# Kernel optimization log

Measured on AMD Instinct MI355X. Metric: run time of the kernel, lower is better.

Reference implementation:

```python
import jax, jax.numpy as jnp
import numpy as np

B, Q, C, H, D, E, I = 8, 256, 192, 20, 64, 1500, 5120
HID = H * D  # 1280
EPS = 1e-5
SCALE = D ** -0.5


def _linear(x, w, b):
    return jnp.einsum('bsh,oh->bso', x, w) + b


def _layernorm(x, w, b):
    xf = x.astype(jnp.float32)
    mu = jnp.mean(xf, axis=-1, keepdims=True)
    var = jnp.mean(jnp.square(xf - mu), axis=-1, keepdims=True)
    return ((xf - mu) * jax.lax.rsqrt(var + EPS) * w + b).astype(x.dtype)


def _heads(x):  # [B,S,HID] -> [B,H,S,D]
    return x.reshape(B, -1, H, D).transpose(0, 2, 1, 3)


def setup_inputs() -> dict:
    key = jax.random.key(0)
    ks = jax.random.split(key, 24)
    s = 0.02
    inp = {
        'hidden_states': jax.random.normal(ks[0], (B, Q, HID), jnp.float32),
        'mask': jnp.zeros((B, 1, Q, Q + C), jnp.float32),
        'past_key': jax.random.normal(ks[1], (B, H, C, D), jnp.float32),
        'past_value': jax.random.normal(ks[2], (B, H, C, D), jnp.float32),
        'cross_key': jax.random.normal(ks[3], (B, H, E, D), jnp.float32),
        'cross_value': jax.random.normal(ks[4], (B, H, E, D), jnp.float32),
        'q_w': jax.random.normal(ks[5], (HID, HID), jnp.float32) * s,
        'q_b': jnp.zeros((HID,), jnp.float32),
        'k_w': jax.random.normal(ks[6], (HID, HID), jnp.float32) * s,
        'k_b': jnp.zeros((HID,), jnp.float32),
        'v_w': jax.random.normal(ks[7], (HID, HID), jnp.float32) * s,
        'v_b': jnp.zeros((HID,), jnp.float32),
        'o_w': jax.random.normal(ks[8], (HID, HID), jnp.float32) * s,
        'o_b': jnp.zeros((HID,), jnp.float32),
        'cq_w': jax.random.normal(ks[9], (HID, HID), jnp.float32) * s,
        'cq_b': jnp.zeros((HID,), jnp.float32),
        'co_w': jax.random.normal(ks[10], (HID, HID), jnp.float32) * s,
        'co_b': jnp.zeros((HID,), jnp.float32),
        'up_w': jax.random.normal(ks[11], (I, HID), jnp.float32) * s,
        'up_b': jnp.zeros((I,), jnp.float32),
        'down_w': jax.random.normal(ks[12], (HID, I), jnp.float32) * s,
        'down_b': jnp.zeros((HID,), jnp.float32),
        'ln1_w': jnp.ones((HID,), jnp.float32),
        'ln1_b': jnp.zeros((HID,), jnp.float32),
        'ln2_w': jnp.ones((HID,), jnp.float32),
        'ln2_b': jnp.zeros((HID,), jnp.float32),
        'ln3_w': jnp.ones((HID,), jnp.float32),
        'ln3_b': jnp.zeros((HID,), jnp.float32),
    }
    return inp


def reference(hidden_states, mask, past_key, past_value, cross_key, cross_value,
              q_w, q_b, k_w, k_b, v_w, v_b, o_w, o_b,
              cq_w, cq_b, co_w, co_b, up_w, up_b, down_w, down_b,
              ln1_w, ln1_b, ln2_w, ln2_b, ln3_w, ln3_b):
    # ---- self-attention block ----
    residual = hidden_states
    x = _layernorm(hidden_states, ln1_w, ln1_b)
    q = _heads(_linear(x, q_w, q_b) * SCALE)          # [B,H,Q,D]
    k_new = _heads(_linear(x, k_w, k_b))              # [B,H,Q,D]
    v_new = _heads(_linear(x, v_w, v_b))
    k = jnp.concatenate([past_key, k_new], axis=2)    # [B,H,C+Q,D]
    v = jnp.concatenate([past_value, v_new], axis=2)
    scores = jnp.einsum('bhqd,bhkd->bhqk', q, k) + mask
    attn = jnp.einsum('bhqk,bhkd->bhqd', jax.nn.softmax(scores, axis=-1), v)
    attn = attn.transpose(0, 2, 1, 3).reshape(B, Q, HID)
    attn_out = _linear(attn, o_w, o_b)
    present_key = k[:, :, Q:, :]
    present_value = v[:, :, Q:, :]
    h = residual + attn_out
    # ---- cross-attention block ----
    residual = h
    x = _layernorm(h, ln2_w, ln2_b)
    cq = _heads(_linear(x, cq_w, cq_b) * SCALE)       # [B,H,Q,D]
    cscores = jnp.einsum('bhqd,bhkd->bhqk', cq, cross_key)
    cattn = jnp.einsum('bhqk,bhkd->bhqd', jax.nn.softmax(cscores, axis=-1), cross_value)
    cattn = cattn.transpose(0, 2, 1, 3).reshape(B, Q, HID)
    h = residual + _linear(cattn, co_w, co_b)
    # ---- MLP block ----
    residual = h
    x = _layernorm(h, ln3_w, ln3_b)
    up = _linear(x, up_w, up_b)
    mlp_out = _linear(jax.nn.gelu(up, approximate=False), down_w, down_b)
    h = residual + mlp_out
    return (h, present_key, present_value)
```

## Files before the change

kernel.cpp:

```cpp
#include <hip/hip_runtime.h>
#include <math.h>

#define Bc   8
#define Qn   256
#define Cn   192
#define Hn   20
#define Dn   64
#define En   1500
#define In   5120
#define HIDn 1280
#define BQ   2048
#define KSELF 448
#define S1   (BQ*HIDn)
#define WSZ  (HIDn*HIDn)

typedef __attribute__((ext_vector_type(8))) short bf16x8;
typedef __attribute__((ext_vector_type(4))) float f32x4;

__device__ __forceinline__ short f2bf(float f) {
  union { float f; unsigned u; } x; x.f = f;
  unsigned r = x.u + 0x7fffu + ((x.u >> 16) & 1u);
  return (short)(r >> 16);
}
__device__ __forceinline__ float bf2f(short s) {
  union { unsigned u; float f; } x; x.u = ((unsigned)(unsigned short)s) << 16;
  return x.f;
}
__device__ __forceinline__ void gload16(const short* g, short* l) {
  __builtin_amdgcn_global_load_lds(
      (const __attribute__((address_space(1))) void*)g,
      (__attribute__((address_space(3))) void*)l, 16, 0, 0);
}

__global__ __launch_bounds__(256) void convert_all(
    const float* q, const float* k, const float* v, const float* o,
    const float* cq, const float* co, const float* up, const float* dn,
    short* wq, short* wk, short* wv, short* wo,
    short* wcq, short* wco, short* wup, short* wdn)
{
  const float* src; short* dst; int n;
  switch (blockIdx.y) {
    case 0: src = q;  dst = wq;  n = WSZ; break;
    case 1: src = k;  dst = wk;  n = WSZ; break;
    case 2: src = v;  dst = wv;  n = WSZ; break;
    case 3: src = o;  dst = wo;  n = WSZ; break;
    case 4: src = cq; dst = wcq; n = WSZ; break;
    case 5: src = co; dst = wco; n = WSZ; break;
    case 6: src = up; dst = wup; n = HIDn * In; break;
    default: src = dn; dst = wdn; n = HIDn * In; break;
  }
  const int i = (blockIdx.x * 256 + threadIdx.x) * 8;
  if (i >= n) return;
  const float4 a = *reinterpret_cast<const float4*>(src + i);
  const float4 b = *reinterpret_cast<const float4*>(src + i + 4);
  bf16x8 t;
  t[0] = f2bf(a.x); t[1] = f2bf(a.y); t[2] = f2bf(a.z); t[3] = f2bf(a.w);
  t[4] = f2bf(b.x); t[5] = f2bf(b.y); t[6] = f2bf(b.z); t[7] = f2bf(b.w);
  *reinterpret_cast<bf16x8*>(dst + i) = t;
}

__global__ __launch_bounds__(256) void layernorm_k(
    const float* __restrict__ in, const float* __restrict__ w,
    const float* __restrict__ b, short* __restrict__ out)
{
  const int row = blockIdx.x;
  const float* x = in + (size_t)row * HIDn;
  float v[5], s = 0.f, s2 = 0.f;
#pragma unroll
  for (int i = 0; i < 5; ++i) {
    float t = x[threadIdx.x + 256 * i];
    v[i] = t; s += t; s2 += t * t;
  }
#pragma unroll
  for (int off = 1; off < 64; off <<= 1) {
    s  += __shfl_xor(s,  off, 64);
    s2 += __shfl_xor(s2, off, 64);
  }
  __shared__ float red[8];
  const int wave = threadIdx.x >> 6, lane = threadIdx.x & 63;
  if (lane == 0) { red[wave] = s; red[wave + 4] = s2; }
  __syncthreads();
  s  = red[0] + red[1] + red[2] + red[3];
  s2 = red[4] + red[5] + red[6] + red[7];
  const float mu  = s / HIDn;
  const float var = s2 / HIDn - mu * mu;
  const float rs  = rsqrtf(var + 1e-5f);
#pragma unroll
  for (int i = 0; i < 5; ++i) {
    const int c = threadIdx.x + 256 * i;
    out[(size_t)row * HIDn + c] = f2bf((v[i] - mu) * rs * w[c] + b[c]);
  }
}

template<int BM, int BN, int MODE>
__global__ __launch_bounds__(256) void gemm_bk64(
    const short* __restrict__ A, const short* __restrict__ W,
    const float* __restrict__ bias, const float* __restrict__ resid,
    void* __restrict__ out0, void* __restrict__ out1, void* __restrict__ out2,
    const float* __restrict__ b1, const float* __restrict__ b2,
    int N, int K, int LDK, float scale)
{
  constexpr int FM = BM / 32, FN = BN / 32;
  __shared__ __align__(16) short Alds[BM * 64];
  __shared__ __align__(16) short Blds[BN * 64];

  const int GX = gridDim.x, GY = gridDim.y;
  int lid = blockIdx.x + GX * (blockIdx.y + GY * blockIdx.z);
  const int cpx = (GX * GY * gridDim.z) >> 3;
  lid = (lid & 7) * cpx + (lid >> 3);
  const int bx = lid % GX;
  const int by = (lid / GX) % GY;
  const int bz = lid / (GX * GY);

  const int tid = threadIdx.x, lane = tid & 63, wave = tid >> 6;
  const int wr = wave >> 1, wc = wave & 1;
  const int m0 = bx * BM, n0 = by * BN;
  const int lr = lane & 15;
  const int kc = (lane >> 4) * 8;
  const size_t koff = (size_t)bz * K;

  f32x4 acc[FM][FN];
#pragma unroll
  for (int mi = 0; mi < FM; ++mi)
#pragma unroll
    for (int ni = 0; ni < FN; ++ni)
      acc[mi][ni] = (f32x4){0.f, 0.f, 0.f, 0.f};

  const int nk = K >> 6;
  for (int kt = 0; kt < nk; ++kt) {
    const int k0 = kt << 6;
#pragma unroll
    for (int j = 0; j < BM / 32; ++j) {
      const int i = wave + 4 * j;
      const int rb = i >> 1, kk = i & 1;
      gload16(A + (size_t)(m0 + rb * 16 + lr) * LDK + koff + k0 + kk * 32 + kc,
              &Alds[i * 512]);
    }
#pragma unroll
    for (int j = 0; j < BN / 32; ++j) {
      const int i = wave + 4 * j;
      const int rb = i >> 1, kk = i & 1;
      gload16(W + (size_t)(n0 + rb * 16 + lr) * LDK + koff + k0 + kk * 32 + kc,
              &Blds[i * 512]);
    }
    __syncthreads();
    bf16x8 af[2][FM], bfv[2][FN];
#pragma unroll
    for (int kk = 0; kk < 2; ++kk) {
#pragma unroll
      for (int mi = 0; mi < FM; ++mi)
        af[kk][mi] = *reinterpret_cast<const bf16x8*>(
            &Alds[((wr * FM + mi) * 2 + kk) * 512 + lane * 8]);
#pragma unroll
      for (int ni = 0; ni < FN; ++ni)
        bfv[kk][ni] = *reinterpret_cast<const bf16x8*>(
            &Blds[((wc * FN + ni) * 2 + kk) * 512 + lane * 8]);
    }
#pragma unroll
    for (int kk = 0; kk < 2; ++kk)
#pragma unroll
      for (int mi = 0; mi < FM; ++mi)
#pragma unroll
        for (int ni = 0; ni < FN; ++ni)
          acc[mi][ni] = __builtin_amdgcn_mfma_f32_16x16x32_bf16(
              af[kk][mi], bfv[kk][ni], acc[mi][ni], 0, 0, 0);
    __syncthreads();
  }

  const int cn = lane & 15;
  const int rb = (lane >> 4) * 4;
#pragma unroll
  for (int mi = 0; mi < FM; ++mi)
#pragma unroll
    for (int ni = 0; ni < FN; ++ni)
#pragma unroll
      for (int j = 0; j < 4; ++j) {
        const int row = m0 + wr * (BM / 2) + mi * 16 + rb + j;
        const int col = n0 + wc * (BN / 2) + ni * 16 + cn;
        const float a = acc[mi][ni][j];
        if (MODE == 0) {
          ((float*)out0)[(size_t)row * N + col] =
              a + bias[col] + resid[(size_t)row * N + col];
        } else if (MODE == 1) {
          ((short*)out0)[(size_t)row * N + col] = f2bf((a + bias[col]) * scale);
        } else if (MODE == 2) {
          float t = a + bias[col];
          t = 0.5f * t * (1.f + erff(t * 0.70710678118654752f));
          ((short*)out0)[(size_t)row * N + col] = f2bf(t);
        } else if (MODE == 3) {
          const int rg  = n0 / 1280;
          const int cl  = col - rg * 1280;
          short* op     = rg == 0 ? (short*)out0 : rg == 1 ? (short*)out1 : (short*)out2;
          const float* bp = rg == 0 ? bias : rg == 1 ? b1 : b2;
          const float sc  = rg == 0 ? 0.125f : 1.f;
          op[(size_t)row * 1280 + cl] = f2bf((a + bp[cl]) * sc);
        } else {
          float* op = bz == 0 ? (float*)out0 : (float*)out1;
          op[(size_t)row * N + col] = a;
        }
      }
}

__global__ __launch_bounds__(256) void reduce_down(
    const float* __restrict__ p0, const float* __restrict__ p1,
    const float* __restrict__ resid, const float* __restrict__ bias,
    float* __restrict__ out)
{
  const size_t i = ((size_t)blockIdx.x * 256 + threadIdx.x) * 4;
  if (i >= (size_t)S1) return;
  const int col = (int)(i % HIDn);
  const float4 a = *reinterpret_cast<const float4*>(p0 + i);
  const float4 b = *reinterpret_cast<const float4*>(p1 + i);
  const float4 r = *reinterpret_cast<const float4*>(resid + i);
  const float4 bi = *reinterpret_cast<const float4*>(bias + col);
  float4 o;
  o.x = a.x + b.x + r.x + bi.x;
  o.y = a.y + b.y + r.y + bi.y;
  o.z = a.z + b.z + r.z + bi.z;
  o.w = a.w + b.w + r.w + bi.w;
  *reinterpret_cast<float4*>(out + i) = o;
}

template<bool HASMASK>
__global__ __launch_bounds__(256) void attn_mfma(
    const short* __restrict__ Qb, const float* __restrict__ Kp,
    const float* __restrict__ Vp, const short* __restrict__ Kn,
    const short* __restrict__ Vn, const float* __restrict__ mask,
    short* __restrict__ Ob, int Cp, int KT)
{
  const int orig = blockIdx.x;
  const int idx  = (orig & 7) * 80 + (orig >> 3);
  const int qt = idx & 3;
  const int h  = (idx >> 2) % Hn;
  const int b  = idx / (4 * Hn);
  const int tid = threadIdx.x, lane = tid & 63, wave = tid >> 6;
  const int q0 = qt * 64;
  const int cn = lane & 15;
  const int hg = lane >> 4;
  const int rb = hg * 4;

  __shared__ __align__(16) short k_s[64][72];
  __shared__ __align__(16) short vt_s[64][72];
  __shared__ __align__(16) short p_s[4][16][72];

  bf16x8 aq[2];
  {
    const short* qrow = Qb + (size_t)(b * Qn + q0 + wave * 16 + cn) * HIDn + h * 64;
    aq[0] = *reinterpret_cast<const bf16x8*>(qrow + hg * 8);
    aq[1] = *reinterpret_cast<const bf16x8*>(qrow + 32 + hg * 8);
  }

  float mrun[4] = {-1e30f, -1e30f, -1e30f, -1e30f};
  float lrun[4] = {0.f, 0.f, 0.f, 0.f};
  f32x4 oacc[4];
#pragma unroll
  for (int t = 0; t < 4; ++t) oacc[t] = (f32x4){0.f, 0.f, 0.f, 0.f};

  const int nchunk = (KT + 63) >> 6;
  for (int ci = 0; ci < nchunk; ++ci) {
    const int c0 = ci * 64;
    for (int i = tid; i < 64 * 8; i += 256) {
      const int key = i >> 3, d8 = (i & 7) * 8;
      const int gk = c0 + key;
      bf16x8 kv8 = (bf16x8)0, vv8 = (bf16x8)0;
      if (gk < KT) {
        if (gk < Cp) {
          const size_t off = (((size_t)b * Hn + h) * (size_t)Cp + gk) * 64 + d8;
          const float4 ka = *reinterpret_cast<const float4*>(Kp + off);
          const float4 kb = *reinterpret_cast<const float4*>(Kp + off + 4);
          const float4 va = *reinterpret_cast<const float4*>(Vp + off);
          const float4 vb = *reinterpret_cast<const float4*>(Vp + off + 4);
          kv8[0] = f2bf(ka.x); kv8[1] = f2bf(ka.y); kv8[2] = f2bf(ka.z); kv8[3] = f2bf(ka.w);
          kv8[4] = f2bf(kb.x); kv8[5] = f2bf(kb.y); kv8[6] = f2bf(kb.z); kv8[7] = f2bf(kb.w);
          vv8[0] = f2bf(va.x); vv8[1] = f2bf(va.y); vv8[2] = f2bf(va.z); vv8[3] = f2bf(va.w);
          vv8[4] = f2bf(vb.x); vv8[5] = f2bf(vb.y); vv8[6] = f2bf(vb.z); vv8[7] = f2bf(vb.w);
        } else {
          const size_t off = (size_t)(b * Qn + (gk - Cp)) * HIDn + h * 64 + d8;
          kv8 = *reinterpret_cast<const bf16x8*>(Kn + off);
          vv8 = *reinterpret_cast<const bf16x8*>(Vn + off);
        }
      }
      *reinterpret_cast<bf16x8*>(&k_s[key][d8]) = kv8;
      const int g = key >> 3, o = key & 7, f = (d8 >> 3) & 7;
#pragma unroll
      for (int j = 0; j < 8; ++j)
        vt_s[d8 + j][((g ^ f) << 3) | o] = vv8[j];
    }
    __syncthreads();

    f32x4 sacc[4];
#pragma unroll
    for (int t = 0; t < 4; ++t) sacc[t] = (f32x4){0.f, 0.f, 0.f, 0.f};
#pragma unroll
    for (int t = 0; t < 4; ++t)
#pragma unroll
      for (int kk = 0; kk < 2; ++kk) {
        const bf16x8 bk = *reinterpret_cast<const bf16x8*>(&k_s[t * 16 + cn][kk * 32 + hg * 8]);
        sacc[t] = __builtin_amdgcn_mfma_f32_16x16x32_bf16(aq[kk], bk, sacc[t], 0, 0, 0);
      }

    float sc[4][4];
#pragma unroll
    for (int t = 0; t < 4; ++t) {
      const int key = c0 + t * 16 + cn;
      const bool valid = key < KT;
#pragma unroll
      for (int j = 0; j < 4; ++j) {
        float v = sacc[t][j];
        if (HASMASK && valid)
          v += mask[((size_t)(b * Qn) + q0 + wave * 16 + rb + j) * KT + key];
        sc[t][j] = valid ? v : -1e30f;
      }
    }

#pragma unroll
    for (int j = 0; j < 4; ++j) {
      float mx = fmaxf(fmaxf(sc[0][j], sc[1][j]), fmaxf(sc[2][j], sc[3][j]));
#pragma unroll
      for (int off = 1; off < 16; off <<= 1) mx = fmaxf(mx, __shfl_xor(mx, off, 64));
      const float mnew  = fmaxf(mrun[j], mx);
      const float alpha = __expf(mrun[j] - mnew);
      float ps = 0.f;
#pragma unroll
      for (int t = 0; t < 4; ++t) {
        const float p = __expf(sc[t][j] - mnew);
        sc[t][j] = p; ps += p;
      }
#pragma unroll
      for (int off = 1; off < 16; off <<= 1) ps += __shfl_xor(ps, off, 64);
      lrun[j] = lrun[j] * alpha + ps;
      mrun[j] = mnew;
#pragma unroll
      for (int t = 0; t < 4; ++t) oacc[t][j] *= alpha;
    }

#pragma unroll
    for (int t = 0; t < 4; ++t)
#pragma unroll
      for (int j = 0; j < 4; ++j)
        p_s[wave][rb + j][t * 16 + cn] = f2bf(sc[t][j]);

    const bf16x8 ap0 = *reinterpret_cast<const bf16x8*>(&p_s[wave][cn][hg * 8]);
    const bf16x8 ap1 = *reinterpret_cast<const bf16x8*>(&p_s[wave][cn][32 + hg * 8]);
#pragma unroll
    for (int t = 0; t < 4; ++t) {
      const int d  = t * 16 + cn;
      const int fd = (d >> 3) & 7;
      const bf16x8 bv0 = *reinterpret_cast<const bf16x8*>(&vt_s[d][((hg)     ^ fd) << 3]);
      const bf16x8 bv1 = *reinterpret_cast<const bf16x8*>(&vt_s[d][((4 + hg) ^ fd) << 3]);
      oacc[t] = __builtin_amdgcn_mfma_f32_16x16x32_bf16(ap0, bv0, oacc[t], 0, 0, 0);
      oacc[t] = __builtin_amdgcn_mfma_f32_16x16x32_bf16(ap1, bv1, oacc[t], 0, 0, 0);
    }
    __syncthreads();
  }

#pragma unroll
  for (int t = 0; t < 4; ++t)
#pragma unroll
    for (int j = 0; j < 4; ++j)
      Ob[(size_t)(b * Qn + q0 + wave * 16 + rb + j) * HIDn + h * 64 + t * 16 + cn] =
          f2bf(oacc[t][j] / lrun[j]);
}

__global__ __launch_bounds__(256) void copy_present(
    const short* __restrict__ kn, const short* __restrict__ vn,
    float* __restrict__ outk, float* __restrict__ outv)
{
  const int idx = blockIdx.x * 256 + threadIdx.x;
  if (idx >= Bc * Hn * Cn * 8) return;
  const int d8 = (idx & 7) * 8;
  int t = idx >> 3;
  const int c = t % Cn; t /= Cn;
  const int h = t % Hn;
  const int b = t / Hn;
  const size_t src = (size_t)(b * Qn + (Qn - Cn) + c) * HIDn + h * 64 + d8;
  const size_t dst = (((size_t)b * Hn + h) * Cn + c) * 64 + d8;
  const bf16x8 kv = *reinterpret_cast<const bf16x8*>(kn + src);
  const bf16x8 vv = *reinterpret_cast<const bf16x8*>(vn + src);
#pragma unroll
  for (int j = 0; j < 8; ++j) {
    outk[dst + j] = bf2f(kv[j]);
    outv[dst + j] = bf2f(vv[j]);
  }
}

extern "C" void kernel_launch(void* const* d_in, const int* in_sizes, int n_in,
                              void* d_out, int out_size, void* d_ws, size_t ws_size,
                              hipStream_t stream)
{
  const float* hidden  = (const float*)d_in[0];
  const float* mask    = (const float*)d_in[1];
  const float* past_k  = (const float*)d_in[2];
  const float* past_v  = (const float*)d_in[3];
  const float* cross_k = (const float*)d_in[4];
  const float* cross_v = (const float*)d_in[5];
  const float* q_w  = (const float*)d_in[6];  const float* q_b  = (const float*)d_in[7];
  const float* k_w  = (const float*)d_in[8];  const float* k_b  = (const float*)d_in[9];
  const float* v_w  = (const float*)d_in[10]; const float* v_b  = (const float*)d_in[11];
  const float* o_w  = (const float*)d_in[12]; const float* o_b  = (const float*)d_in[13];
  const float* cq_w = (const float*)d_in[14]; const float* cq_b = (const float*)d_in[15];
  const float* co_w = (const float*)d_in[16]; const float* co_b = (const float*)d_in[17];
  const float* up_w = (const float*)d_in[18]; const float* up_b = (const float*)d_in[19];
  const float* dn_w = (const float*)d_in[20]; const float* dn_b = (const float*)d_in[21];
  const float* ln1w = (const float*)d_in[22]; const float* ln1b = (const float*)d_in[23];
  const float* ln2w = (const float*)d_in[24]; const float* ln2b = (const float*)d_in[25];
  const float* ln3w = (const float*)d_in[26]; const float* ln3b = (const float*)d_in[27];

  short* wq  = (short*)d_ws;
  short* wk  = wq  + (size_t)WSZ;
  short* wv  = wk  + (size_t)WSZ;
  short* wo  = wv  + (size_t)WSZ;
  short* wcq = wo  + (size_t)WSZ;
  short* wco = wcq + (size_t)WSZ;
  short* wup = wco + (size_t)WSZ;
  short* wdn = wup + (size_t)HIDn * In;
  short* xb  = wdn + (size_t)HIDn * In;
  short* qb  = xb  + (size_t)S1;
  short* kb  = qb  + (size_t)S1;
  short* vb  = kb  + (size_t)S1;
  short* ab  = vb  + (size_t)S1;
  short* upa = ab  + (size_t)S1;
  float* h1  = (float*)(upa + (size_t)BQ * In);
  float* h2  = h1 + (size_t)S1;
  float* p0  = (float*)qb;
  float* p1  = (float*)vb;

  float* out_h  = (float*)d_out;
  float* out_pk = out_h + (size_t)S1;
  float* out_pv = out_pk + (size_t)(Bc * Hn * Cn * Dn);

  const dim3 blk(256);
  const dim3 gconv(3200, 8);
  const dim3 gqkv(32, 30);
  const dim3 g64(32, 20);
  const dim3 gup(32, 40);
  const dim3 gdn(32, 20, 2);
  const dim3 gattn(640);

  convert_all<<<gconv, blk, 0, stream>>>(q_w, k_w, v_w, o_w, cq_w, co_w, up_w, dn_w,
                                         wq, wk, wv, wo, wcq, wco, wup, wdn);
  layernorm_k<<<BQ, blk, 0, stream>>>(hidden, ln1w, ln1b, xb);
  gemm_bk64<64, 128, 3><<<gqkv, blk, 0, stream>>>(xb, wq, q_b, nullptr,
      qb, kb, vb, k_b, v_b, 3840, HIDn, HIDn, 1.f);
  copy_present<<<(Bc * Hn * Cn * 8 + 255) / 256, blk, 0, stream>>>(kb, vb, out_pk, out_pv);
  attn_mfma<true><<<gattn, blk, 0, stream>>>(qb, past_k, past_v, kb, vb, mask, ab, Cn, KSELF);
  gemm_bk64<64, 64, 0><<<g64, blk, 0, stream>>>(ab, wo, o_b, hidden,
      h1, nullptr, nullptr, nullptr, nullptr, HIDn, HIDn, HIDn, 1.f);
  layernorm_k<<<BQ, blk, 0, stream>>>(h1, ln2w, ln2b, xb);
  gemm_bk64<64, 64, 1><<<g64, blk, 0, stream>>>(xb, wcq, cq_b, nullptr,
      qb, nullptr, nullptr, nullptr, nullptr, HIDn, HIDn, HIDn, 0.125f);
  attn_mfma<false><<<gattn, blk, 0, stream>>>(qb, cross_k, cross_v,
      (const short*)nullptr, (const short*)nullptr, nullptr, ab, En, En);
  gemm_bk64<64, 64, 0><<<g64, blk, 0, stream>>>(ab, wco, co_b, h1,
      h2, nullptr, nullptr, nullptr, nullptr, HIDn, HIDn, HIDn, 1.f);
  layernorm_k<<<BQ, blk, 0, stream>>>(h2, ln3w, ln3b, xb);
  gemm_bk64<64, 128, 2><<<gup, blk, 0, stream>>>(xb, wup, up_b, nullptr,
      upa, nullptr, nullptr, nullptr, nullptr, In, HIDn, HIDn, 1.f);
  gemm_bk64<64, 64, 4><<<gdn, blk, 0, stream>>>(upa, wdn, nullptr, nullptr,
      p0, p1, nullptr, nullptr, nullptr, HIDn, In / 2, In, 1.f);
  reduce_down<<<(S1 / 4 + 255) / 256, blk, 0, stream>>>(p0, p1, h2, dn_b, out_h);
}
```

Before: 541.7 us.

## Pre-convert attention K/V to bf16, lazily rescale softmax, enlarge GEMM tiles

Two new prep kernels convert the cross-attention and self-attention K/V to contiguous bf16 buffers; the cross buffer is padded to 1536 keys. The attention kernel can then load bf16 tiles directly instead of repeating the fp32-to-bf16 conversion and branchy gathers in every query-tile block. The online softmax now rescales only when the running max grows by more than 8, which skips most exp/multiply rescale work. GEMM tiles grow from BM=64 to BM=128, the XCD block-swizzle is removed, and h2 is stored in the output buffer. The cost is an extra round trip through memory for the converted K/V and fewer GEMM blocks per launch.

```diff
diff --git a/kernel.cpp b/kernel.cpp
--- a/kernel.cpp
+++ b/kernel.cpp
@@ -11,8 +11,10 @@
 #define HIDn 1280
 #define BQ   2048
 #define KSELF 448
+#define EPAD 1536
 #define S1   (BQ*HIDn)
 #define WSZ  (HIDn*HIDn)
+#define BH   (Bc*Hn)
 
 typedef __attribute__((ext_vector_type(8))) short bf16x8;
 typedef __attribute__((ext_vector_type(4))) float f32x4;
@@ -30,6 +32,14 @@
   __builtin_amdgcn_global_load_lds(
       (const __attribute__((address_space(1))) void*)g,
       (__attribute__((address_space(3))) void*)l, 16, 0, 0);
+}
+__device__ __forceinline__ bf16x8 cvt8(const float* p) {
+  const float4 a = *reinterpret_cast<const float4*>(p);
+  const float4 b = *reinterpret_cast<const float4*>(p + 4);
+  bf16x8 t;
+  t[0] = f2bf(a.x); t[1] = f2bf(a.y); t[2] = f2bf(a.z); t[3] = f2bf(a.w);
+  t[4] = f2bf(b.x); t[5] = f2bf(b.y); t[6] = f2bf(b.z); t[7] = f2bf(b.w);
+  return t;
 }
 
 __global__ __launch_bounds__(256) void convert_all(
@@ -51,12 +61,53 @@
   }
   const int i = (blockIdx.x * 256 + threadIdx.x) * 8;
   if (i >= n) return;
-  const float4 a = *reinterpret_cast<const float4*>(src + i);
-  const float4 b = *reinterpret_cast<const float4*>(src + i + 4);
-  bf16x8 t;
-  t[0] = f2bf(a.x); t[1] = f2bf(a.y); t[2] = f2bf(a.z); t[3] = f2bf(a.w);
-  t[4] = f2bf(b.x); t[5] = f2bf(b.y); t[6] = f2bf(b.z); t[7] = f2bf(b.w);
-  *reinterpret_cast<bf16x8*>(dst + i) = t;
+  *reinterpret_cast<bf16x8*>(dst + i) = cvt8(src + i);
+}
+
+__global__ __launch_bounds__(256) void prep_cross(
+    const float* __restrict__ K, const float* __restrict__ V,
+    short* __restrict__ Kc, short* __restrict__ Vc)
+{
+  const size_t idx = (size_t)blockIdx.x * 256 + threadIdx.x;
+  const int d8 = (int)(idx & 7) * 8;
+  const size_t t = idx >> 3;
+  const int key = (int)(t % EPAD);
+  const int bh  = (int)(t / EPAD);
+  bf16x8 kv = (bf16x8)0, vv = (bf16x8)0;
+  if (key < En) {
+    const size_t off = ((size_t)bh * En + key) * 64 + d8;
+    kv = cvt8(K + off);
+    vv = cvt8(V + off);
+  }
+  const size_t dst = ((size_t)bh * EPAD + key) * 64 + d8;
+  *reinterpret_cast<bf16x8*>(Kc + dst) = kv;
+  *reinterpret_cast<bf16x8*>(Vc + dst) = vv;
+}
+
+__global__ __launch_bounds__(256) void prep_self(
+    const float* __restrict__ Kp, const float* __restrict__ Vp,
+    const short* __restrict__ kn, const short* __restrict__ vn,
+    short* __restrict__ Kc, short* __restrict__ Vc)
+{
+  const size_t idx = (size_t)blockIdx.x * 256 + threadIdx.x;
+  const int d8 = (int)(idx & 7) * 8;
+  const size_t t = idx >> 3;
+  const int key = (int)(t % KSELF);
+  const int bh  = (int)(t / KSELF);
+  bf16x8 kv, vv;
+  if (key < Cn) {
+    const size_t off = ((size_t)bh * Cn + key) * 64 + d8;
+    kv = cvt8(Kp + off);
+    vv = cvt8(Vp + off);
+  } else {
+    const int b = bh / Hn, h = bh % Hn;
+    const size_t off = ((size_t)(b * Qn + (key - Cn))) * HIDn + h * 64 + d8;
+    kv = *reinterpret_cast<const bf16x8*>(kn + off);
+    vv = *reinterpret_cast<const bf16x8*>(vn + off);
+  }
+  const size_t dst = ((size_t)bh * KSELF + key) * 64 + d8;
+  *reinterpret_cast<bf16x8*>(Kc + dst) = kv;
+  *reinterpret_cast<bf16x8*>(Vc + dst) = vv;
 }
 
 __global__ __launch_bounds__(256) void layernorm_k(
@@ -103,18 +154,10 @@
   constexpr int FM = BM / 32, FN = BN / 32;
   __shared__ __align__(16) short Alds[BM * 64];
   __shared__ __align__(16) short Blds[BN * 64];
-
-  const int GX = gridDim.x, GY = gridDim.y;
-  int lid = blockIdx.x + GX * (blockIdx.y + GY * blockIdx.z);
-  const int cpx = (GX * GY * gridDim.z) >> 3;
-  lid = (lid & 7) * cpx + (lid >> 3);
-  const int bx = lid % GX;
-  const int by = (lid / GX) % GY;
-  const int bz = lid / (GX * GY);
-
   const int tid = threadIdx.x, lane = tid & 63, wave = tid >> 6;
   const int wr = wave >> 1, wc = wave & 1;
-  const int m0 = bx * BM, n0 = by * BN;
+  const int m0 = blockIdx.x * BM, n0 = blockIdx.y * BN;
+  const int bz = blockIdx.z;
   const int lr = lane & 15;
   const int kc = (lane >> 4) * 8;
   const size_t koff = (size_t)bz * K;
@@ -223,16 +266,16 @@
 
 template<bool HASMASK>
 __global__ __launch_bounds__(256) void attn_mfma(
-    const short* __restrict__ Qb, const float* __restrict__ Kp,
-    const float* __restrict__ Vp, const short* __restrict__ Kn,
-    const short* __restrict__ Vn, const float* __restrict__ mask,
-    short* __restrict__ Ob, int Cp, int KT)
+    const short* __restrict__ Qb, const short* __restrict__ Kc,
+    const short* __restrict__ Vc, const float* __restrict__ mask,
+    short* __restrict__ Ob, int PADK, int KT)
 {
   const int orig = blockIdx.x;
   const int idx  = (orig & 7) * 80 + (orig >> 3);
   const int qt = idx & 3;
   const int h  = (idx >> 2) % Hn;
   const int b  = idx / (4 * Hn);
+  const int bh = b * Hn + h;
   const int tid = threadIdx.x, lane = tid & 63, wave = tid >> 6;
   const int q0 = qt * 64;
   const int cn = lane & 15;
@@ -256,35 +299,22 @@
 #pragma unroll
   for (int t = 0; t < 4; ++t) oacc[t] = (f32x4){0.f, 0.f, 0.f, 0.f};
 
-  const int nchunk = (KT + 63) >> 6;
+  const int nchunk = PADK >> 6;
   for (int ci = 0; ci < nchunk; ++ci) {
     const int c0 = ci * 64;
-    for (int i = tid; i < 64 * 8; i += 256) {
+    const short* kbase = Kc + ((size_t)bh * PADK + c0) * 64;
+    const short* vbase = Vc + ((size_t)bh * PADK + c0) * 64;
+#pragma unroll
+    for (int r = 0; r < 2; ++r) {
+      const int i = tid + r * 256;
       const int key = i >> 3, d8 = (i & 7) * 8;
-      const int gk = c0 + key;
-      bf16x8 kv8 = (bf16x8)0, vv8 = (bf16x8)0;
-      if (gk < KT) {
-        if (gk < Cp) {
-          const size_t off = (((size_t)b * Hn + h) * (size_t)Cp + gk) * 64 + d8;
-          const float4 ka = *reinterpret_cast<const float4*>(Kp + off);
-          const float4 kb = *reinterpret_cast<const float4*>(Kp + off + 4);
-          const float4 va = *reinterpret_cast<const float4*>(Vp + off);
-          const float4 vb = *reinterpret_cast<const float4*>(Vp + off + 4);
-          kv8[0] = f2bf(ka.x); kv8[1] = f2bf(ka.y); kv8[2] = f2bf(ka.z); kv8[3] = f2bf(ka.w);
-          kv8[4] = f2bf(kb.x); kv8[5] = f2bf(kb.y); kv8[6] = f2bf(kb.z); kv8[7] = f2bf(kb.w);
-          vv8[0] = f2bf(va.x); vv8[1] = f2bf(va.y); vv8[2] = f2bf(va.z); vv8[3] = f2bf(va.w);
-          vv8[4] = f2bf(vb.x); vv8[5] = f2bf(vb.y); vv8[6] = f2bf(vb.z); vv8[7] = f2bf(vb.w);
-        } else {
-          const size_t off = (size_t)(b * Qn + (gk - Cp)) * HIDn + h * 64 + d8;
-          kv8 = *reinterpret_cast<const bf16x8*>(Kn + off);
-          vv8 = *reinterpret_cast<const bf16x8*>(Vn + off);
-        }
-      }
-      *reinterpret_cast<bf16x8*>(&k_s[key][d8]) = kv8;
-      const int g = key >> 3, o = key & 7, f = (d8 >> 3) & 7;
-#pragma unroll
-      for (int j = 0; j < 8; ++j)
-        vt_s[d8 + j][((g ^ f) << 3) | o] = vv8[j];
+      const bf16x8 kv = *reinterpret_cast<const bf16x8*>(kbase + key * 64 + d8);
+      const bf16x8 vv = *reinterpret_cast<const bf16x8*>(vbase + key * 64 + d8);
+      *reinterpret_cast<bf16x8*>(&k_s[key][d8]) = kv;
+      const int g = key >> 3, o = key & 7, f = i & 7;
+      const int col = ((g ^ f) << 3) | o;
+#pragma unroll
+      for (int j = 0; j < 8; ++j) vt_s[d8 + j][col] = vv[j];
     }
     __syncthreads();
 
@@ -318,20 +348,22 @@
       float mx = fmaxf(fmaxf(sc[0][j], sc[1][j]), fmaxf(sc[2][j], sc[3][j]));
 #pragma unroll
       for (int off = 1; off < 16; off <<= 1) mx = fmaxf(mx, __shfl_xor(mx, off, 64));
-      const float mnew  = fmaxf(mrun[j], mx);
-      const float alpha = __expf(mrun[j] - mnew);
+      if (mx > mrun[j] + 8.f) {
+        const float alpha = __expf(mrun[j] - mx);
+        lrun[j] *= alpha;
+#pragma unroll
+        for (int t = 0; t < 4; ++t) oacc[t][j] *= alpha;
+        mrun[j] = mx;
+      }
       float ps = 0.f;
 #pragma unroll
       for (int t = 0; t < 4; ++t) {
-        const float p = __expf(sc[t][j] - mnew);
+        const float p = __expf(sc[t][j] - mrun[j]);
         sc[t][j] = p; ps += p;
       }
 #pragma unroll
       for (int off = 1; off < 16; off <<= 1) ps += __shfl_xor(ps, off, 64);
-      lrun[j] = lrun[j] * alpha + ps;
-      mrun[j] = mnew;
-#pragma unroll
-      for (int t = 0; t < 4; ++t) oacc[t][j] *= alpha;
+      lrun[j] += ps;
     }
 
 #pragma unroll
@@ -419,44 +451,50 @@
   short* kb  = qb  + (size_t)S1;
   short* vb  = kb  + (size_t)S1;
   short* ab  = vb  + (size_t)S1;
-  short* upa = ab  + (size_t)S1;
-  float* h1  = (float*)(upa + (size_t)BQ * In);
-  float* h2  = h1 + (size_t)S1;
+  short* U   = ab  + (size_t)S1;
+  short* ksb = U;
+  short* vsb = U + (size_t)BH * KSELF * 64;
+  short* upa = U;
+  short* kcc = U + (size_t)BQ * In;
+  short* vcc = kcc + (size_t)BH * EPAD * 64;
+  float* h1  = (float*)(vcc + (size_t)BH * EPAD * 64);
   float* p0  = (float*)qb;
   float* p1  = (float*)vb;
 
   float* out_h  = (float*)d_out;
   float* out_pk = out_h + (size_t)S1;
   float* out_pv = out_pk + (size_t)(Bc * Hn * Cn * Dn);
+  float* h2 = out_h;
 
   const dim3 blk(256);
   const dim3 gconv(3200, 8);
-  const dim3 gqkv(32, 30);
-  const dim3 g64(32, 20);
-  const dim3 gup(32, 40);
-  const dim3 gdn(32, 20, 2);
+  const dim3 gqkv(16, 30);
+  const dim3 gn64(16, 20);
+  const dim3 gup(16, 40);
+  const dim3 gdn(16, 20, 2);
   const dim3 gattn(640);
 
   convert_all<<<gconv, blk, 0, stream>>>(q_w, k_w, v_w, o_w, cq_w, co_w, up_w, dn_w,
                                          wq, wk, wv, wo, wcq, wco, wup, wdn);
+  prep_cross<<<(BH * EPAD * 8) / 256, blk, 0, stream>>>(cross_k, cross_v, kcc, vcc);
   layernorm_k<<<BQ, blk, 0, stream>>>(hidden, ln1w, ln1b, xb);
-  gemm_bk64<64, 128, 3><<<gqkv, blk, 0, stream>>>(xb, wq, q_b, nullptr,
+  gemm_bk64<128, 128, 3><<<gqkv, blk, 0, stream>>>(xb, wq, q_b, nullptr,
       qb, kb, vb, k_b, v_b, 3840, HIDn, HIDn, 1.f);
   copy_present<<<(Bc * Hn * Cn * 8 + 255) / 256, blk, 0, stream>>>(kb, vb, out_pk, out_pv);
-  attn_mfma<true><<<gattn, blk, 0, stream>>>(qb, past_k, past_v, kb, vb, mask, ab, Cn, KSELF);
-  gemm_bk64<64, 64, 0><<<g64, blk, 0, stream>>>(ab, wo, o_b, hidden,
+  prep_self<<<(BH * KSELF * 8) / 256, blk, 0, stream>>>(past_k, past_v, kb, vb, ksb, vsb);
+  attn_mfma<true><<<gattn, blk, 0, stream>>>(qb, ksb, vsb, mask, ab, KSELF, KSELF);
+  gemm_bk64<128, 64, 0><<<gn64, blk, 0, stream>>>(ab, wo, o_b, hidden,
       h1, nullptr, nullptr, nullptr, nullptr, HIDn, HIDn, HIDn, 1.f);
   layernorm_k<<<BQ, blk, 0, stream>>>(h1, ln2w, ln2b, xb);
-  gemm_bk64<64, 64, 1><<<g64, blk, 0, stream>>>(xb, wcq, cq_b, nullptr,
+  gemm_bk64<128, 64, 1><<<gn64, blk, 0, stream>>>(xb, wcq, cq_b, nullptr,
       qb, nullptr, nullptr, nullptr, nullptr, HIDn, HIDn, HIDn, 0.125f);
-  attn_mfma<false><<<gattn, blk, 0, stream>>>(qb, cross_k, cross_v,
-      (const short*)nullptr, (const short*)nullptr, nullptr, ab, En, En);
-  gemm_bk64<64, 64, 0><<<g64, blk, 0, stream>>>(ab, wco, co_b, h1,
+  attn_mfma<false><<<gattn, blk, 0, stream>>>(qb, kcc, vcc, nullptr, ab, EPAD, En);
+  gemm_bk64<128, 64, 0><<<gn64, blk, 0, stream>>>(ab, wco, co_b, h1,
       h2, nullptr, nullptr, nullptr, nullptr, HIDn, HIDn, HIDn, 1.f);
   layernorm_k<<<BQ, blk, 0, stream>>>(h2, ln3w, ln3b, xb);
-  gemm_bk64<64, 128, 2><<<gup, blk, 0, stream>>>(xb, wup, up_b, nullptr,
+  gemm_bk64<128, 128, 2><<<gup, blk, 0, stream>>>(xb, wup, up_b, nullptr,
       upa, nullptr, nullptr, nullptr, nullptr, In, HIDn, HIDn, 1.f);
-  gemm_bk64<64, 64, 4><<<gdn, blk, 0, stream>>>(upa, wdn, nullptr, nullptr,
+  gemm_bk64<128, 64, 4><<<gdn, blk, 0, stream>>>(upa, wdn, nullptr, nullptr,
       p0, p1, nullptr, nullptr, nullptr, HIDn, In / 2, In, 1.f);
   reduce_down<<<(S1 / 4 + 255) / 256, blk, 0, stream>>>(p0, p1, h2, dn_b, out_h);
 }
```

After: 539.7 us. About the same (-0.4%).
